# Kernel optimization log

Measured on AMD Instinct MI355X. Metric: run time of the kernel, lower is better.

Reference implementation:

```python
import jax, jax.numpy as jnp
import numpy as np

FEAT_DIM = 2048
HID = 256
N = 1024
NUM_CLASSES = 16
BN_EPS = 1e-5


def _batchnorm(x, gamma, beta):
    # training-mode BatchNorm1d: per-batch mean, biased variance
    m = x.mean(axis=0)
    v = x.var(axis=0)
    return gamma * (x - m) / jnp.sqrt(v + BN_EPS) + beta


def setup_inputs() -> dict:
    key = jax.random.key(0)
    ks = jax.random.split(key, 12)
    s1 = 1.0 / np.sqrt(FEAT_DIM)
    s2 = 1.0 / np.sqrt(HID)
    s3 = 1.0 / np.sqrt(2 * HID)
    return {
        "features": jax.random.normal(ks[0], (N, FEAT_DIM), dtype=jnp.float32),
        "labels": jax.random.randint(ks[1], (N,), 0, NUM_CLASSES, dtype=jnp.int32),
        # semantic disentangler
        "W1": jax.random.normal(ks[2], (FEAT_DIM, HID), dtype=jnp.float32) * s1,
        "b1": jnp.zeros((HID,), jnp.float32),
        "g1": jnp.ones((HID,), jnp.float32),
        "bt1": jnp.zeros((HID,), jnp.float32),
        "W2": jax.random.normal(ks[3], (HID, HID), dtype=jnp.float32) * s2,
        "b2": jnp.zeros((HID,), jnp.float32),
        "g2": jnp.ones((HID,), jnp.float32),
        "bt2": jnp.zeros((HID,), jnp.float32),
        # edge network: Linear(2H -> H), Linear(H -> 1)
        "We1": jax.random.normal(ks[4], (2 * HID, HID), dtype=jnp.float32) * s3,
        "bwe1": jnp.zeros((HID,), jnp.float32),
        "We2": jax.random.normal(ks[5], (HID, 1), dtype=jnp.float32) * s2,
        "bwe2": jnp.zeros((1,), jnp.float32),
    }


def reference(features, labels, W1, b1, g1, bt1, W2, b2, g2, bt2,
              We1, bwe1, We2, bwe2):
    # semantic disentangler: (Linear -> BN -> ReLU) x2
    h = jax.nn.relu(_batchnorm(features @ W1 + b1, g1, bt1))
    di = jax.nn.relu(_batchnorm(h @ W2 + b2, g2, bt2))  # [N, H]

    # EdgeNetwork all-pairs: Linear on concat([f_i, f_j]) splits into two GEMMs
    hi = di @ We1[:HID]   # [N, H] contribution of node i (first half of concat)
    hj = di @ We1[HID:]   # [N, H] contribution of node j (second half)
    pair = jax.nn.relu(hi[:, None, :] + hj[None, :, :] + bwe1)  # [N, N, H]
    logits = pair @ We2[:, 0] + bwe2[0]                          # [N, N]
    same_label = labels[:, None] == labels[None, :]
    off_diag = ~jnp.eye(N, dtype=bool)
    edge_weights = jnp.where(same_label & off_diag,
                             jax.nn.sigmoid(logits), 0.0)        # [N, N]

    # update_node_features: f_i + sum_j w_ij f_j / sum_j w_ij (if wsum > 0)
    weighted_sum = edge_weights @ di                 # [N, H] (w_ii == 0)
    wsum = edge_weights.sum(axis=1, keepdims=True)   # [N, 1]
    denom = jnp.where(wsum > 0, wsum, 1.0)
    updated = di + jnp.where(wsum > 0, weighted_sum / denom, 0.0)
    return updated
```

## Files before the change

### kernel.cpp

```cpp
#include <hip/hip_runtime.h>
#include <math.h>

#define N_PTS 1024
#define HID   256
#define FEAT  2048

typedef short bf16x8 __attribute__((ext_vector_type(8)));
typedef float f32x4  __attribute__((ext_vector_type(4)));

__device__ inline ushort f2bf(float f) {
    union { float f; unsigned u; } v; v.f = f;
    unsigned r = v.u + 0x7fff + ((v.u >> 16) & 1);
    return (ushort)(r >> 16);
}

__global__ __launch_bounds__(256) void prep(
    const float* __restrict__ features, const float* __restrict__ W1,
    const float* __restrict__ W2, const float* __restrict__ We1,
    ushort* __restrict__ Af, ushort* __restrict__ W1T,
    ushort* __restrict__ W2T, ushort* __restrict__ WeT,
    float* __restrict__ stats)
{
    const int tid = threadIdx.x;
    int b = blockIdx.x;
    if (b < 512) {
        if (b == 300)
            ((float4*)stats)[tid] = make_float4(0.f, 0.f, 0.f, 0.f);
        #pragma unroll
        for (int q = 0; q < 2; q++) {
            const size_t g = (size_t)b * 256 + tid + (size_t)q * 131072;
            float4 v0 = ((const float4*)features)[g * 2];
            float4 v1 = ((const float4*)features)[g * 2 + 1];
            bf16x8 o;
            o[0] = (short)f2bf(v0.x); o[1] = (short)f2bf(v0.y);
            o[2] = (short)f2bf(v0.z); o[3] = (short)f2bf(v0.w);
            o[4] = (short)f2bf(v1.x); o[5] = (short)f2bf(v1.y);
            o[6] = (short)f2bf(v1.z); o[7] = (short)f2bf(v1.w);
            ((bf16x8*)Af)[g] = o;
        }
        return;
    }
    __shared__ ushort Ts[64 * 72];
    const float* src; ushort* dst; int K;
    b -= 512;
    if (b < 128)      { src = W1;  dst = W1T; K = 2048; }
    else if (b < 144) { b -= 128; src = W2;  dst = W2T; K = 256; }
    else              { b -= 144; src = We1; dst = WeT; K = 512; }
    const int k0 = (b >> 2) * 64;
    const int n0 = (b & 3) * 64;
    #pragma unroll
    for (int p = 0; p < 4; p++) {
        const int c  = p * 256 + tid;
        const int r  = c >> 4;
        const int cq = c & 15;
        float4 v = *(const float4*)&src[(size_t)(k0 + r) * 256 + n0 + cq * 4];
        Ts[(cq * 4 + 0) * 72 + r] = f2bf(v.x);
        Ts[(cq * 4 + 1) * 72 + r] = f2bf(v.y);
        Ts[(cq * 4 + 2) * 72 + r] = f2bf(v.z);
        Ts[(cq * 4 + 3) * 72 + r] = f2bf(v.w);
    }
    __syncthreads();
    #pragma unroll
    for (int p = 0; p < 2; p++) {
        const int c    = p * 256 + tid;
        const int row  = c >> 3;
        const int col8 = c & 7;
        *(bf16x8*)&dst[(size_t)(n0 + row) * K + k0 + col8 * 8] =
            *(bf16x8*)&Ts[row * 72 + col8 * 8];
    }
}

__global__ __launch_bounds__(256) void gemm1p(
    const ushort* __restrict__ A, const ushort* __restrict__ B,
    float* __restrict__ Cp)
{
    __shared__ ushort As[64 * 72];
    __shared__ ushort Bs[64 * 72];
    const int tid  = threadIdx.x;
    const int lane = tid & 63;
    const int wave = tid >> 6;
    const int wy = wave >> 1, wx = wave & 1;
    const int quad = lane >> 4, l16 = lane & 15;
    const int mBase = blockIdx.y * 64;
    const int nBase = blockIdx.x * 64;
    const int kBeg  = blockIdx.z * 256;
    float* C = Cp + (size_t)blockIdx.z * (N_PTS * HID);

    f32x4 acc[2][2] = {};
    for (int ks = kBeg; ks < kBeg + 256; ks += 64) {
        #pragma unroll
        for (int p = 0; p < 2; p++) {
            const int c    = p * 256 + tid;
            const int row  = c >> 3;
            const int col8 = c & 7;
            *(bf16x8*)&As[row * 72 + col8 * 8] =
                *(const bf16x8*)&A[(size_t)(mBase + row) * FEAT + ks + col8 * 8];
            *(bf16x8*)&Bs[row * 72 + col8 * 8] =
                *(const bf16x8*)&B[(size_t)(nBase + row) * FEAT + ks + col8 * 8];
        }
        __syncthreads();
        #pragma unroll
        for (int kt = 0; kt < 64; kt += 32) {
            bf16x8 af[2], bfr[2];
            #pragma unroll
            for (int mi = 0; mi < 2; mi++)
                af[mi] = *(bf16x8*)&As[(wy * 32 + mi * 16 + l16) * 72 + kt + quad * 8];
            #pragma unroll
            for (int ni = 0; ni < 2; ni++)
                bfr[ni] = *(bf16x8*)&Bs[(wx * 32 + ni * 16 + l16) * 72 + kt + quad * 8];
            #pragma unroll
            for (int mi = 0; mi < 2; mi++)
                #pragma unroll
                for (int ni = 0; ni < 2; ni++)
                    acc[mi][ni] = __builtin_amdgcn_mfma_f32_16x16x32_bf16(
                        af[mi], bfr[ni], acc[mi][ni], 0, 0, 0);
        }
        __syncthreads();
    }
    #pragma unroll
    for (int mi = 0; mi < 2; mi++)
        #pragma unroll
        for (int ni = 0; ni < 2; ni++)
            #pragma unroll
            for (int e = 0; e < 4; e++) {
                const int gm = mBase + wy * 32 + mi * 16 + quad * 4 + e;
                const int gn = nBase + wx * 32 + ni * 16 + l16;
                C[(size_t)gm * HID + gn] = acc[mi][ni][e];
            }
}

__global__ __launch_bounds__(256) void reduce_stats(
    const float* __restrict__ Xp, float* __restrict__ X,
    float* __restrict__ sum, float* __restrict__ sq)
{
    const int c = threadIdx.x;
    const int r0 = blockIdx.x * 4;
    float s = 0.f, q = 0.f;
    for (int r = r0; r < r0 + 4; ++r) {
        float v = 0.f;
        #pragma unroll
        for (int z = 0; z < 8; z++)
            v += Xp[(size_t)z * (N_PTS * HID) + r * HID + c];
        X[r * HID + c] = v;
        s += v;
        q = fmaf(v, v, q);
    }
    unsafeAtomicAdd(&sum[c], s);
    unsafeAtomicAdd(&sq[c], q);
}

__global__ __launch_bounds__(256) void gemm2_fused(
    const float* __restrict__ A , const ushort* __restrict__ B ,
    float* __restrict__ C ,
    const float* __restrict__ sum1, const float* __restrict__ sq1,
    const float* __restrict__ g1, const float* __restrict__ bt1,
    float* __restrict__ sum2, float* __restrict__ sq2)
{
    __shared__ ushort As[64 * 72];
    __shared__ ushort Bs[64 * 72];
    __shared__ float sscale[HID];
    __shared__ float sshift[HID];
    __shared__ float csum[64];
    __shared__ float csq[64];
    const int tid  = threadIdx.x;
    const int lane = tid & 63;
    const int wave = tid >> 6;
    const int wy = wave >> 1, wx = wave & 1;
    const int quad = lane >> 4, l16 = lane & 15;
    const int mBase = blockIdx.y * 64;
    const int nBase = blockIdx.x * 64;

    {
        float m   = sum1[tid] * (1.f / 1024.f);
        float var = fmaf(-m, m, sq1[tid] * (1.f / 1024.f));
        float rstd = rsqrtf(var + 1e-5f);
        float sc = g1[tid] * rstd;
        sscale[tid] = sc;
        sshift[tid] = fmaf(-m, sc, bt1[tid]);
    }
    if (tid < 64) { csum[tid] = 0.f; csq[tid] = 0.f; }
    __syncthreads();

    f32x4 acc[2][2] = {};
    for (int ks = 0; ks < HID; ks += 64) {
        #pragma unroll
        for (int p = 0; p < 4; p++) {
            const int c  = p * 256 + tid;
            const int r  = c >> 4;
            const int cq = c & 15;
            const int k0 = ks + cq * 4;
            float4 av = *(const float4*)&A[(size_t)(mBase + r) * HID + k0];
            float v0 = fmaxf(fmaf(sscale[k0 + 0], av.x, sshift[k0 + 0]), 0.f);
            float v1 = fmaxf(fmaf(sscale[k0 + 1], av.y, sshift[k0 + 1]), 0.f);
            float v2 = fmaxf(fmaf(sscale[k0 + 2], av.z, sshift[k0 + 2]), 0.f);
            float v3 = fmaxf(fmaf(sscale[k0 + 3], av.w, sshift[k0 + 3]), 0.f);
            ushort4 ao;
            ao.x = f2bf(v0); ao.y = f2bf(v1); ao.z = f2bf(v2); ao.w = f2bf(v3);
            *(ushort4*)&As[r * 72 + cq * 4] = ao;
        }
        #pragma unroll
        for (int p = 0; p < 2; p++) {
            const int c    = p * 256 + tid;
            const int row  = c >> 3;
            const int col8 = c & 7;
            *(bf16x8*)&Bs[row * 72 + col8 * 8] =
                *(const bf16x8*)&B[(size_t)(nBase + row) * HID + ks + col8 * 8];
        }
        __syncthreads();
        #pragma unroll
        for (int kt = 0; kt < 64; kt += 32) {
            bf16x8 af[2], bfr[2];
            #pragma unroll
            for (int mi = 0; mi < 2; mi++)
                af[mi] = *(bf16x8*)&As[(wy * 32 + mi * 16 + l16) * 72 + kt + quad * 8];
            #pragma unroll
            for (int ni = 0; ni < 2; ni++)
                bfr[ni] = *(bf16x8*)&Bs[(wx * 32 + ni * 16 + l16) * 72 + kt + quad * 8];
            #pragma unroll
            for (int mi = 0; mi < 2; mi++)
                #pragma unroll
                for (int ni = 0; ni < 2; ni++)
                    acc[mi][ni] = __builtin_amdgcn_mfma_f32_16x16x32_bf16(
                        af[mi], bfr[ni], acc[mi][ni], 0, 0, 0);
        }
        __syncthreads();
    }

    float s[2] = {0.f, 0.f}, q[2] = {0.f, 0.f};
    #pragma unroll
    for (int mi = 0; mi < 2; mi++)
        #pragma unroll
        for (int ni = 0; ni < 2; ni++)
            #pragma unroll
            for (int e = 0; e < 4; e++) {
                const int gm = mBase + wy * 32 + mi * 16 + quad * 4 + e;
                const int gn = nBase + wx * 32 + ni * 16 + l16;
                float v = acc[mi][ni][e];
                C[(size_t)gm * HID + gn] = v;
                s[ni] += v;
                q[ni] = fmaf(v, v, q[ni]);
            }
    #pragma unroll
    for (int ni = 0; ni < 2; ni++) {
        float sv = s[ni], qv = q[ni];
        sv += __shfl_xor(sv, 16, 64); sv += __shfl_xor(sv, 32, 64);
        qv += __shfl_xor(qv, 16, 64); qv += __shfl_xor(qv, 32, 64);
        if (quad == 0) {
            atomicAdd(&csum[wx * 32 + ni * 16 + l16], sv);
            atomicAdd(&csq [wx * 32 + ni * 16 + l16], qv);
        }
    }
    __syncthreads();
    if (tid < 64) {
        unsafeAtomicAdd(&sum2[nBase + tid], csum[tid]);
        unsafeAtomicAdd(&sq2 [nBase + tid], csq[tid]);
    }
}

__global__ __launch_bounds__(256) void gemm_dual_bn(
    const float* __restrict__ A , const ushort* __restrict__ WeT,
    float* __restrict__ C1 , float* __restrict__ C2 ,
    const float* __restrict__ sum2, const float* __restrict__ sq2,
    const float* __restrict__ g2, const float* __restrict__ bt2,
    float* __restrict__ di)
{
    __shared__ ushort As[64 * 72];
    __shared__ ushort Bs[64 * 72];
    __shared__ float sscale[HID];
    __shared__ float sshift[HID];
    const int tid  = threadIdx.x;
    const int lane = tid & 63;
    const int wave = tid >> 6;
    const int wy = wave >> 1, wx = wave & 1;
    const int quad = lane >> 4, l16 = lane & 15;
    const int mBase = blockIdx.y * 64;
    const int nBase = blockIdx.x * 64;
    const int half  = blockIdx.z;
    float* C = half ? C2 : C1;
    const bool writeDi = (blockIdx.x == 0) && (half == 0);

    {
        float m   = sum2[tid] * (1.f / 1024.f);
        float var = fmaf(-m, m, sq2[tid] * (1.f / 1024.f));
        float rstd = rsqrtf(var + 1e-5f);
        float sc = g2[tid] * rstd;
        sscale[tid] = sc;
        sshift[tid] = fmaf(-m, sc, bt2[tid]);
    }
    __syncthreads();

    f32x4 acc[2][2] = {};
    for (int ks = 0; ks < HID; ks += 64) {
        #pragma unroll
        for (int p = 0; p < 4; p++) {
            const int c  = p * 256 + tid;
            const int r  = c >> 4;
            const int cq = c & 15;
            const int k0 = ks + cq * 4;
            float4 av = *(const float4*)&A[(size_t)(mBase + r) * HID + k0];
            float v0 = fmaxf(fmaf(sscale[k0 + 0], av.x, sshift[k0 + 0]), 0.f);
            float v1 = fmaxf(fmaf(sscale[k0 + 1], av.y, sshift[k0 + 1]), 0.f);
            float v2 = fmaxf(fmaf(sscale[k0 + 2], av.z, sshift[k0 + 2]), 0.f);
            float v3 = fmaxf(fmaf(sscale[k0 + 3], av.w, sshift[k0 + 3]), 0.f);
            if (writeDi)
                *(float4*)&di[(size_t)(mBase + r) * HID + k0] =
                    make_float4(v0, v1, v2, v3);
            ushort4 ao;
            ao.x = f2bf(v0); ao.y = f2bf(v1); ao.z = f2bf(v2); ao.w = f2bf(v3);
            *(ushort4*)&As[r * 72 + cq * 4] = ao;
        }
        #pragma unroll
        for (int p = 0; p < 2; p++) {
            const int c    = p * 256 + tid;
            const int row  = c >> 3;
            const int col8 = c & 7;
            *(bf16x8*)&Bs[row * 72 + col8 * 8] =
                *(const bf16x8*)&WeT[(size_t)(nBase + row) * 512 + half * 256 + ks + col8 * 8];
        }
        __syncthreads();
        #pragma unroll
        for (int kt = 0; kt < 64; kt += 32) {
            bf16x8 af[2], bfr[2];
            #pragma unroll
            for (int mi = 0; mi < 2; mi++)
                af[mi] = *(bf16x8*)&As[(wy * 32 + mi * 16 + l16) * 72 + kt + quad * 8];
            #pragma unroll
            for (int ni = 0; ni < 2; ni++)
                bfr[ni] = *(bf16x8*)&Bs[(wx * 32 + ni * 16 + l16) * 72 + kt + quad * 8];
            #pragma unroll
            for (int mi = 0; mi < 2; mi++)
                #pragma unroll
                for (int ni = 0; ni < 2; ni++)
                    acc[mi][ni] = __builtin_amdgcn_mfma_f32_16x16x32_bf16(
                        af[mi], bfr[ni], acc[mi][ni], 0, 0, 0);
        }
        __syncthreads();
    }
    #pragma unroll
    for (int mi = 0; mi < 2; mi++)
        #pragma unroll
        for (int ni = 0; ni < 2; ni++)
            #pragma unroll
            for (int e = 0; e < 4; e++) {
                const int gm = mBase + wy * 32 + mi * 16 + quad * 4 + e;
                const int gn = nBase + wx * 32 + ni * 16 + l16;
                C[(size_t)gm * HID + gn] = acc[mi][ni][e];
            }
}

__global__ __launch_bounds__(256) void pair_update2(
    const float* __restrict__ di, const float* __restrict__ hi,
    const float* __restrict__ hj, const float* __restrict__ bwe1,
    const float* __restrict__ We2, const float* __restrict__ bwe2,
    const int* __restrict__ labels, float* __restrict__ out)
{
    __shared__ int   slab[N_PTS];
    __shared__ int   list[N_PTS];
    __shared__ int   cnt;
    __shared__ float sacc[16][HID];
    __shared__ float swsum[16];
    const int i   = blockIdx.x;
    const int tid = threadIdx.x;
    const int pid = tid >> 4;
    const int l16 = tid & 15;

    if (tid == 0) cnt = 0;
    for (int t = tid; t < N_PTS; t += 256) slab[t] = labels[t];
    __syncthreads();
    const int myLab = slab[i];
    for (int t = tid; t < N_PTS; t += 256)
        if (slab[t] == myLab && t != i) list[atomicAdd(&cnt, 1)] = t;
    __syncthreads();
    const int n = cnt;

    const float4* hip4 = (const float4*)(hi + (size_t)i * HID) + l16 * 4;
    const float4* bw4  = (const float4*)bwe1 + l16 * 4;
    const float4* w24  = (const float4*)We2  + l16 * 4;
    float4 hb[4], w2[4];
    #pragma unroll
    for (int s = 0; s < 4; s++) {
        float4 a = hip4[s], b = bw4[s];
        hb[s] = make_float4(a.x + b.x, a.y + b.y, a.z + b.z, a.w + b.w);
        w2[s] = w24[s];
    }
    const float b2 = bwe2[0];

    float4 acc[4] = {};
    float wloc = 0.f;
    const int rounds = (n + 15) >> 4;
    for (int r = 0; r < rounds; ++r) {
        const int idx = r * 16 + pid;
        const bool valid = idx < n;
        const int jj = valid ? list[idx] : i;
        const float4* hv4 = (const float4*)(hj + (size_t)jj * HID) + l16 * 4;
        float4 hv[4];
        #pragma unroll
        for (int s = 0; s < 4; s++) hv[s] = hv4[s];
        float p = 0.f;
        #pragma unroll
        for (int s = 0; s < 4; s++) {
            p = fmaf(fmaxf(hb[s].x + hv[s].x, 0.f), w2[s].x, p);
            p = fmaf(fmaxf(hb[s].y + hv[s].y, 0.f), w2[s].y, p);
            p = fmaf(fmaxf(hb[s].z + hv[s].z, 0.f), w2[s].z, p);
            p = fmaf(fmaxf(hb[s].w + hv[s].w, 0.f), w2[s].w, p);
        }
        p += __shfl_xor(p, 1, 64);
        p += __shfl_xor(p, 2, 64);
        p += __shfl_xor(p, 4, 64);
        p += __shfl_xor(p, 8, 64);
        const float w = valid ? 1.f / (1.f + expf(-(p + b2))) : 0.f;
        const float4* dv4 = (const float4*)(di + (size_t)jj * HID) + l16 * 4;
        #pragma unroll
        for (int s = 0; s < 4; s++) {
            float4 d = dv4[s];
            acc[s].x = fmaf(w, d.x, acc[s].x);
            acc[s].y = fmaf(w, d.y, acc[s].y);
            acc[s].z = fmaf(w, d.z, acc[s].z);
            acc[s].w = fmaf(w, d.w, acc[s].w);
        }
        if (l16 == 0) wloc += w;
    }
    #pragma unroll
    for (int s = 0; s < 4; s++)
        ((float4*)&sacc[pid][l16 * 16])[s] = acc[s];
    if (l16 == 0) swsum[pid] = wloc;
    __syncthreads();

    float at = 0.f;
    #pragma unroll
    for (int g = 0; g < 16; g++) at += sacc[g][tid];
    float wt = 0.f;
    #pragma unroll
    for (int g = 0; g < 16; g++) wt += swsum[g];
    const float dval = di[(size_t)i * HID + tid];
    out[(size_t)i * HID + tid] = dval + (wt > 0.f ? at / wt : 0.f);
}

extern "C" void kernel_launch(void* const* d_in, const int* in_sizes, int n_in,
                              void* d_out, int out_size, void* d_ws, size_t ws_size,
                              hipStream_t stream)
{
    const float* features = (const float*)d_in[0];
    const int*   labels   = (const int*)d_in[1];
    const float* W1   = (const float*)d_in[2];
    const float* g1   = (const float*)d_in[4];
    const float* bt1  = (const float*)d_in[5];
    const float* W2   = (const float*)d_in[6];
    const float* g2   = (const float*)d_in[8];
    const float* bt2  = (const float*)d_in[9];
    const float* We1  = (const float*)d_in[10];
    const float* bwe1 = (const float*)d_in[11];
    const float* We2  = (const float*)d_in[12];
    const float* bwe2 = (const float*)d_in[13];
    float* out = (float*)d_out;

    float* ws    = (float*)d_ws;
    float* x1    = ws;
    float* hi    = ws + 262144;
    float* hj    = ws + 524288;
    float* stats = ws + 786432;
    float* x2    = ws + 787456;
    float* di    = ws + 1049600;
    float* x1p   = ws + 1311744;
    ushort* Af   = (ushort*)(ws + 3408896);
    ushort* W1T  = Af + 2097152;
    ushort* W2T  = W1T + 524288;
    ushort* WeT  = W2T + 65536;

    dim3 blk(256);
    prep<<<688, blk, 0, stream>>>(features, W1, W2, We1, Af, W1T, W2T, WeT,
                                  stats);
    gemm1p<<<dim3(4, 16, 8), blk, 0, stream>>>(Af, W1T, x1p);
    reduce_stats<<<256, blk, 0, stream>>>(x1p, x1, stats, stats + 256);
    gemm2_fused<<<dim3(4, 16, 1), blk, 0, stream>>>(x1, W2T, x2,
                                                    stats, stats + 256, g1, bt1,
                                                    stats + 512, stats + 768);
    gemm_dual_bn<<<dim3(4, 16, 2), blk, 0, stream>>>(x2, WeT, hi, hj,
                                                     stats + 512, stats + 768,
                                                     g2, bt2, di);
    pair_update2<<<N_PTS, blk, 0, stream>>>(di, hi, hj, bwe1, We2, bwe2,
                                            labels, out);
}
```

Baseline: 138.4 us.

## Fuse all stages into one persistent kernel with software grid barriers

Replaces the six separate kernel launches with a single persistent 512-block kernel. Stages are separated by an atomic-counter grid barrier, and the counter is reset with a memset before each launch. This is meant to remove per-launch overhead and the gaps between dependent kernels. In exchange, several stages now run on only a subset of blocks while the rest sit idle. The barrier also needs every block to be co-resident, and its spin loop has a timeout that could silently break correctness if that does not hold.

```diff
diff --git a/kernel.cpp b/kernel.cpp
--- a/kernel.cpp
+++ b/kernel.cpp
@@ -4,6 +4,7 @@
 #define N_PTS 1024
 #define HID   256
 #define FEAT  2048
+#define GRID  512
 
 typedef short bf16x8 __attribute__((ext_vector_type(8)));
 typedef float f32x4  __attribute__((ext_vector_type(4)));
@@ -14,21 +15,60 @@
     return (ushort)(r >> 16);
 }
 
-__global__ __launch_bounds__(256) void prep(
-    const float* __restrict__ features, const float* __restrict__ W1,
-    const float* __restrict__ W2, const float* __restrict__ We1,
-    ushort* __restrict__ Af, ushort* __restrict__ W1T,
-    ushort* __restrict__ W2T, ushort* __restrict__ WeT,
-    float* __restrict__ stats)
+__device__ __forceinline__ void gridbar(unsigned* cnt, unsigned target) {
+    __syncthreads();
+    if (threadIdx.x == 0) {
+        __threadfence();
+        __hip_atomic_fetch_add(cnt, 1u, __ATOMIC_ACQ_REL,
+                               __HIP_MEMORY_SCOPE_AGENT);
+        unsigned spins = 0;
+        while (__hip_atomic_load(cnt, __ATOMIC_ACQUIRE,
+                                 __HIP_MEMORY_SCOPE_AGENT) < target) {
+            __builtin_amdgcn_s_sleep(2);
+            if (++spins > (1u << 22)) break;
+        }
+        __threadfence();
+    }
+    __syncthreads();
+}
+
+__global__ __launch_bounds__(256, 2) void fused_all(
+    const float* __restrict__ features, const int* __restrict__ labels,
+    const float* __restrict__ W1, const float* __restrict__ g1,
+    const float* __restrict__ bt1, const float* __restrict__ W2,
+    const float* __restrict__ g2, const float* __restrict__ bt2,
+    const float* __restrict__ We1, const float* __restrict__ bwe1,
+    const float* __restrict__ We2, const float* __restrict__ bwe2,
+    float* __restrict__ out, float* __restrict__ ws)
 {
-    const int tid = threadIdx.x;
-    int b = blockIdx.x;
-    if (b < 512) {
-        if (b == 300)
+    __shared__ __align__(16) unsigned char smem[24704];
+
+    float* x1    = ws;
+    float* hi    = ws + 262144;
+    float* hj    = ws + 524288;
+    float* stats = ws + 786432;
+    float* x2    = ws + 787456;
+    float* di    = ws + 1049600;
+    float* x1p   = ws + 1311744;
+    ushort* Af   = (ushort*)(ws + 3408896);
+    ushort* W1T  = Af + 2097152;
+    ushort* W2T  = W1T + 524288;
+    ushort* WeT  = W2T + 65536;
+    unsigned* bar = (unsigned*)(ws + 4817920);
+
+    const int tid  = threadIdx.x;
+    const int bid  = blockIdx.x;
+    const int lane = tid & 63;
+    const int wave = tid >> 6;
+    const int wy = wave >> 1, wx = wave & 1;
+    const int quad = lane >> 4, l16 = lane & 15;
+
+    {
+        if (bid == 300)
             ((float4*)stats)[tid] = make_float4(0.f, 0.f, 0.f, 0.f);
         #pragma unroll
         for (int q = 0; q < 2; q++) {
-            const size_t g = (size_t)b * 256 + tid + (size_t)q * 131072;
+            const size_t g = (size_t)bid * 256 + tid + (size_t)q * 131072;
             float4 v0 = ((const float4*)features)[g * 2];
             float4 v1 = ((const float4*)features)[g * 2 + 1];
             bf16x8 o;
@@ -38,402 +78,369 @@
             o[6] = (short)f2bf(v1.z); o[7] = (short)f2bf(v1.w);
             ((bf16x8*)Af)[g] = o;
         }
-        return;
-    }
-    __shared__ ushort Ts[64 * 72];
-    const float* src; ushort* dst; int K;
-    b -= 512;
-    if (b < 128)      { src = W1;  dst = W1T; K = 2048; }
-    else if (b < 144) { b -= 128; src = W2;  dst = W2T; K = 256; }
-    else              { b -= 144; src = We1; dst = WeT; K = 512; }
-    const int k0 = (b >> 2) * 64;
-    const int n0 = (b & 3) * 64;
-    #pragma unroll
-    for (int p = 0; p < 4; p++) {
-        const int c  = p * 256 + tid;
-        const int r  = c >> 4;
-        const int cq = c & 15;
-        float4 v = *(const float4*)&src[(size_t)(k0 + r) * 256 + n0 + cq * 4];
-        Ts[(cq * 4 + 0) * 72 + r] = f2bf(v.x);
-        Ts[(cq * 4 + 1) * 72 + r] = f2bf(v.y);
-        Ts[(cq * 4 + 2) * 72 + r] = f2bf(v.z);
-        Ts[(cq * 4 + 3) * 72 + r] = f2bf(v.w);
-    }
-    __syncthreads();
-    #pragma unroll
-    for (int p = 0; p < 2; p++) {
-        const int c    = p * 256 + tid;
-        const int row  = c >> 3;
-        const int col8 = c & 7;
-        *(bf16x8*)&dst[(size_t)(n0 + row) * K + k0 + col8 * 8] =
-            *(bf16x8*)&Ts[row * 72 + col8 * 8];
-    }
-}
-
-__global__ __launch_bounds__(256) void gemm1p(
-    const ushort* __restrict__ A, const ushort* __restrict__ B,
-    float* __restrict__ Cp)
-{
-    __shared__ ushort As[64 * 72];
-    __shared__ ushort Bs[64 * 72];
-    const int tid  = threadIdx.x;
-    const int lane = tid & 63;
-    const int wave = tid >> 6;
-    const int wy = wave >> 1, wx = wave & 1;
-    const int quad = lane >> 4, l16 = lane & 15;
-    const int mBase = blockIdx.y * 64;
-    const int nBase = blockIdx.x * 64;
-    const int kBeg  = blockIdx.z * 256;
-    float* C = Cp + (size_t)blockIdx.z * (N_PTS * HID);
-
-    f32x4 acc[2][2] = {};
-    for (int ks = kBeg; ks < kBeg + 256; ks += 64) {
-        #pragma unroll
-        for (int p = 0; p < 2; p++) {
-            const int c    = p * 256 + tid;
-            const int row  = c >> 3;
-            const int col8 = c & 7;
-            *(bf16x8*)&As[row * 72 + col8 * 8] =
-                *(const bf16x8*)&A[(size_t)(mBase + row) * FEAT + ks + col8 * 8];
-            *(bf16x8*)&Bs[row * 72 + col8 * 8] =
-                *(const bf16x8*)&B[(size_t)(nBase + row) * FEAT + ks + col8 * 8];
-        }
+        if (bid < 176) {
+            ushort* Ts = (ushort*)smem;
+            int b = bid; const float* src; ushort* dst; int K;
+            if (b < 128)      { src = W1;  dst = W1T; K = 2048; }
+            else if (b < 144) { b -= 128; src = W2;  dst = W2T; K = 256; }
+            else              { b -= 144; src = We1; dst = WeT; K = 512; }
+            const int k0 = (b >> 2) * 64;
+            const int n0 = (b & 3) * 64;
+            #pragma unroll
+            for (int p = 0; p < 4; p++) {
+                const int c  = p * 256 + tid;
+                const int r  = c >> 4;
+                const int cq = c & 15;
+                float4 v = *(const float4*)&src[(size_t)(k0 + r) * 256 + n0 + cq * 4];
+                Ts[(cq * 4 + 0) * 72 + r] = f2bf(v.x);
+                Ts[(cq * 4 + 1) * 72 + r] = f2bf(v.y);
+                Ts[(cq * 4 + 2) * 72 + r] = f2bf(v.z);
+                Ts[(cq * 4 + 3) * 72 + r] = f2bf(v.w);
+            }
+            __syncthreads();
+            #pragma unroll
+            for (int p = 0; p < 2; p++) {
+                const int c    = p * 256 + tid;
+                const int row  = c >> 3;
+                const int col8 = c & 7;
+                *(bf16x8*)&dst[(size_t)(n0 + row) * K + k0 + col8 * 8] =
+                    *(bf16x8*)&Ts[row * 72 + col8 * 8];
+            }
+        }
+    }
+    gridbar(bar, 1 * GRID);
+
+    {
+        ushort* As = (ushort*)smem;
+        ushort* Bs = (ushort*)(smem + 9216);
+        const int x = bid & 3, y = (bid >> 2) & 15, z = bid >> 6;
+        const int mBase = y * 64, nBase = x * 64, kBeg = z * 256;
+        float* C = x1p + (size_t)z * (N_PTS * HID);
+        f32x4 acc[2][2] = {};
+        for (int ks = kBeg; ks < kBeg + 256; ks += 64) {
+            #pragma unroll
+            for (int p = 0; p < 2; p++) {
+                const int c    = p * 256 + tid;
+                const int row  = c >> 3;
+                const int col8 = c & 7;
+                *(bf16x8*)&As[row * 72 + col8 * 8] =
+                    *(const bf16x8*)&Af[(size_t)(mBase + row) * FEAT + ks + col8 * 8];
+                *(bf16x8*)&Bs[row * 72 + col8 * 8] =
+                    *(const bf16x8*)&W1T[(size_t)(nBase + row) * FEAT + ks + col8 * 8];
+            }
+            __syncthreads();
+            #pragma unroll
+            for (int kt = 0; kt < 64; kt += 32) {
+                bf16x8 af[2], bfr[2];
+                #pragma unroll
+                for (int mi = 0; mi < 2; mi++)
+                    af[mi] = *(bf16x8*)&As[(wy * 32 + mi * 16 + l16) * 72 + kt + quad * 8];
+                #pragma unroll
+                for (int ni = 0; ni < 2; ni++)
+                    bfr[ni] = *(bf16x8*)&Bs[(wx * 32 + ni * 16 + l16) * 72 + kt + quad * 8];
+                #pragma unroll
+                for (int mi = 0; mi < 2; mi++)
+                    #pragma unroll
+                    for (int ni = 0; ni < 2; ni++)
+                        acc[mi][ni] = __builtin_amdgcn_mfma_f32_16x16x32_bf16(
+                            af[mi], bfr[ni], acc[mi][ni], 0, 0, 0);
+            }
+            __syncthreads();
+        }
+        #pragma unroll
+        for (int mi = 0; mi < 2; mi++)
+            #pragma unroll
+            for (int ni = 0; ni < 2; ni++)
+                #pragma unroll
+                for (int e = 0; e < 4; e++) {
+                    const int gm = mBase + wy * 32 + mi * 16 + quad * 4 + e;
+                    const int gn = nBase + wx * 32 + ni * 16 + l16;
+                    C[(size_t)gm * HID + gn] = acc[mi][ni][e];
+                }
+    }
+    gridbar(bar, 2 * GRID);
+
+    if (bid < 256) {
+        const int c = tid;
+        const int r0 = bid * 4;
+        float s = 0.f, q = 0.f;
+        for (int r = r0; r < r0 + 4; ++r) {
+            float v = 0.f;
+            #pragma unroll
+            for (int z = 0; z < 8; z++)
+                v += x1p[(size_t)z * (N_PTS * HID) + r * HID + c];
+            x1[r * HID + c] = v;
+            s += v;
+            q = fmaf(v, v, q);
+        }
+        unsafeAtomicAdd(&stats[c], s);
+        unsafeAtomicAdd(&stats[256 + c], q);
+    }
+    gridbar(bar, 3 * GRID);
+
+    if (bid < 64) {
+        ushort* As = (ushort*)smem;
+        ushort* Bs = (ushort*)(smem + 9216);
+        float* sscale = (float*)(smem + 18432);
+        float* sshift = (float*)(smem + 19456);
+        float* csum   = (float*)(smem + 20480);
+        float* csq    = (float*)(smem + 20736);
+        const int x = bid & 3, y = bid >> 2;
+        const int mBase = y * 64, nBase = x * 64;
+        {
+            float m   = stats[tid] * (1.f / 1024.f);
+            float var = fmaf(-m, m, stats[256 + tid] * (1.f / 1024.f));
+            float rstd = rsqrtf(var + 1e-5f);
+            float sc = g1[tid] * rstd;
+            sscale[tid] = sc;
+            sshift[tid] = fmaf(-m, sc, bt1[tid]);
+        }
+        if (tid < 64) { csum[tid] = 0.f; csq[tid] = 0.f; }
         __syncthreads();
-        #pragma unroll
-        for (int kt = 0; kt < 64; kt += 32) {
-            bf16x8 af[2], bfr[2];
-            #pragma unroll
-            for (int mi = 0; mi < 2; mi++)
-                af[mi] = *(bf16x8*)&As[(wy * 32 + mi * 16 + l16) * 72 + kt + quad * 8];
+
+        f32x4 acc[2][2] = {};
+        for (int ks = 0; ks < HID; ks += 64) {
+            #pragma unroll
+            for (int p = 0; p < 4; p++) {
+                const int c  = p * 256 + tid;
+                const int r  = c >> 4;
+                const int cq = c & 15;
+                const int k0 = ks + cq * 4;
+                float4 av = *(const float4*)&x1[(size_t)(mBase + r) * HID + k0];
+                float v0 = fmaxf(fmaf(sscale[k0 + 0], av.x, sshift[k0 + 0]), 0.f);
+                float v1 = fmaxf(fmaf(sscale[k0 + 1], av.y, sshift[k0 + 1]), 0.f);
+                float v2 = fmaxf(fmaf(sscale[k0 + 2], av.z, sshift[k0 + 2]), 0.f);
+                float v3 = fmaxf(fmaf(sscale[k0 + 3], av.w, sshift[k0 + 3]), 0.f);
+                ushort4 ao;
+                ao.x = f2bf(v0); ao.y = f2bf(v1); ao.z = f2bf(v2); ao.w = f2bf(v3);
+                *(ushort4*)&As[r * 72 + cq * 4] = ao;
+            }
+            #pragma unroll
+            for (int p = 0; p < 2; p++) {
+                const int c    = p * 256 + tid;
+                const int row  = c >> 3;
+                const int col8 = c & 7;
+                *(bf16x8*)&Bs[row * 72 + col8 * 8] =
+                    *(const bf16x8*)&W2T[(size_t)(nBase + row) * HID + ks + col8 * 8];
+            }
+            __syncthreads();
+            #pragma unroll
+            for (int kt = 0; kt < 64; kt += 32) {
+                bf16x8 af[2], bfr[2];
+                #pragma unroll
+                for (int mi = 0; mi < 2; mi++)
+                    af[mi] = *(bf16x8*)&As[(wy * 32 + mi * 16 + l16) * 72 + kt + quad * 8];
+                #pragma unroll
+                for (int ni = 0; ni < 2; ni++)
+                    bfr[ni] = *(bf16x8*)&Bs[(wx * 32 + ni * 16 + l16) * 72 + kt + quad * 8];
+                #pragma unroll
+                for (int mi = 0; mi < 2; mi++)
+                    #pragma unroll
+                    for (int ni = 0; ni < 2; ni++)
+                        acc[mi][ni] = __builtin_amdgcn_mfma_f32_16x16x32_bf16(
+                            af[mi], bfr[ni], acc[mi][ni], 0, 0, 0);
+            }
+            __syncthreads();
+        }
+        float s[2] = {0.f, 0.f}, q[2] = {0.f, 0.f};
+        #pragma unroll
+        for (int mi = 0; mi < 2; mi++)
             #pragma unroll
             for (int ni = 0; ni < 2; ni++)
-                bfr[ni] = *(bf16x8*)&Bs[(wx * 32 + ni * 16 + l16) * 72 + kt + quad * 8];
-            #pragma unroll
-            for (int mi = 0; mi < 2; mi++)
+                #pragma unroll
+                for (int e = 0; e < 4; e++) {
+                    const int gm = mBase + wy * 32 + mi * 16 + quad * 4 + e;
+                    const int gn = nBase + wx * 32 + ni * 16 + l16;
+                    float v = acc[mi][ni][e];
+                    x2[(size_t)gm * HID + gn] = v;
+                    s[ni] += v;
+                    q[ni] = fmaf(v, v, q[ni]);
+                }
+        #pragma unroll
+        for (int ni = 0; ni < 2; ni++) {
+            float sv = s[ni], qv = q[ni];
+            sv += __shfl_xor(sv, 16, 64); sv += __shfl_xor(sv, 32, 64);
+            qv += __shfl_xor(qv, 16, 64); qv += __shfl_xor(qv, 32, 64);
+            if (quad == 0) {
+                atomicAdd(&csum[wx * 32 + ni * 16 + l16], sv);
+                atomicAdd(&csq [wx * 32 + ni * 16 + l16], qv);
+            }
+        }
+        __syncthreads();
+        if (tid < 64) {
+            unsafeAtomicAdd(&stats[512 + nBase + tid], csum[tid]);
+            unsafeAtomicAdd(&stats[768 + nBase + tid], csq[tid]);
+        }
+    }
+    gridbar(bar, 4 * GRID);
+
+    if (bid < 128) {
+        ushort* As = (ushort*)smem;
+        ushort* Bs = (ushort*)(smem + 9216);
+        float* sscale = (float*)(smem + 18432);
+        float* sshift = (float*)(smem + 19456);
+        const int x = bid & 3, y = (bid >> 2) & 15, half = bid >> 6;
+        const int mBase = y * 64, nBase = x * 64;
+        float* C = half ? hj : hi;
+        const bool writeDi = (x == 0) && (half == 0);
+        {
+            float m   = stats[512 + tid] * (1.f / 1024.f);
+            float var = fmaf(-m, m, stats[768 + tid] * (1.f / 1024.f));
+            float rstd = rsqrtf(var + 1e-5f);
+            float sc = g2[tid] * rstd;
+            sscale[tid] = sc;
+            sshift[tid] = fmaf(-m, sc, bt2[tid]);
+        }
+        __syncthreads();
+
+        f32x4 acc[2][2] = {};
+        for (int ks = 0; ks < HID; ks += 64) {
+            #pragma unroll
+            for (int p = 0; p < 4; p++) {
+                const int c  = p * 256 + tid;
+                const int r  = c >> 4;
+                const int cq = c & 15;
+                const int k0 = ks + cq * 4;
+                float4 av = *(const float4*)&x2[(size_t)(mBase + r) * HID + k0];
+                float v0 = fmaxf(fmaf(sscale[k0 + 0], av.x, sshift[k0 + 0]), 0.f);
+                float v1 = fmaxf(fmaf(sscale[k0 + 1], av.y, sshift[k0 + 1]), 0.f);
+                float v2 = fmaxf(fmaf(sscale[k0 + 2], av.z, sshift[k0 + 2]), 0.f);
+                float v3 = fmaxf(fmaf(sscale[k0 + 3], av.w, sshift[k0 + 3]), 0.f);
+                if (writeDi)
+                    *(float4*)&di[(size_t)(mBase + r) * HID + k0] =
+                        make_float4(v0, v1, v2, v3);
+                ushort4 ao;
+                ao.x = f2bf(v0); ao.y = f2bf(v1); ao.z = f2bf(v2); ao.w = f2bf(v3);
+                *(ushort4*)&As[r * 72 + cq * 4] = ao;
+            }
+            #pragma unroll
+            for (int p = 0; p < 2; p++) {
+                const int c    = p * 256 + tid;
+                const int row  = c >> 3;
+                const int col8 = c & 7;
+                *(bf16x8*)&Bs[row * 72 + col8 * 8] =
+                    *(const bf16x8*)&WeT[(size_t)(nBase + row) * 512 + half * 256 + ks + col8 * 8];
+            }
+            __syncthreads();
+            #pragma unroll
+            for (int kt = 0; kt < 64; kt += 32) {
+                bf16x8 af[2], bfr[2];
+                #pragma unroll
+                for (int mi = 0; mi < 2; mi++)
+                    af[mi] = *(bf16x8*)&As[(wy * 32 + mi * 16 + l16) * 72 + kt + quad * 8];
                 #pragma unroll
                 for (int ni = 0; ni < 2; ni++)
-                    acc[mi][ni] = __builtin_amdgcn_mfma_f32_16x16x32_bf16(
-                        af[mi], bfr[ni], acc[mi][ni], 0, 0, 0);
-        }
-        __syncthreads();
-    }
-    #pragma unroll
-    for (int mi = 0; mi < 2; mi++)
-        #pragma unroll
-        for (int ni = 0; ni < 2; ni++)
-            #pragma unroll
-            for (int e = 0; e < 4; e++) {
-                const int gm = mBase + wy * 32 + mi * 16 + quad * 4 + e;
-                const int gn = nBase + wx * 32 + ni * 16 + l16;
-                C[(size_t)gm * HID + gn] = acc[mi][ni][e];
-            }
-}
-
-__global__ __launch_bounds__(256) void reduce_stats(
-    const float* __restrict__ Xp, float* __restrict__ X,
-    float* __restrict__ sum, float* __restrict__ sq)
-{
-    const int c = threadIdx.x;
-    const int r0 = blockIdx.x * 4;
-    float s = 0.f, q = 0.f;
-    for (int r = r0; r < r0 + 4; ++r) {
-        float v = 0.f;
-        #pragma unroll
-        for (int z = 0; z < 8; z++)
-            v += Xp[(size_t)z * (N_PTS * HID) + r * HID + c];
-        X[r * HID + c] = v;
-        s += v;
-        q = fmaf(v, v, q);
-    }
-    unsafeAtomicAdd(&sum[c], s);
-    unsafeAtomicAdd(&sq[c], q);
-}
-
-__global__ __launch_bounds__(256) void gemm2_fused(
-    const float* __restrict__ A , const ushort* __restrict__ B ,
-    float* __restrict__ C ,
-    const float* __restrict__ sum1, const float* __restrict__ sq1,
-    const float* __restrict__ g1, const float* __restrict__ bt1,
-    float* __restrict__ sum2, float* __restrict__ sq2)
-{
-    __shared__ ushort As[64 * 72];
-    __shared__ ushort Bs[64 * 72];
-    __shared__ float sscale[HID];
-    __shared__ float sshift[HID];
-    __shared__ float csum[64];
-    __shared__ float csq[64];
-    const int tid  = threadIdx.x;
-    const int lane = tid & 63;
-    const int wave = tid >> 6;
-    const int wy = wave >> 1, wx = wave & 1;
-    const int quad = lane >> 4, l16 = lane & 15;
-    const int mBase = blockIdx.y * 64;
-    const int nBase = blockIdx.x * 64;
+                    bfr[ni] = *(bf16x8*)&Bs[(wx * 32 + ni * 16 + l16) * 72 + kt + quad * 8];
+                #pragma unroll
+                for (int mi = 0; mi < 2; mi++)
+                    #pragma unroll
+                    for (int ni = 0; ni < 2; ni++)
+                        acc[mi][ni] = __builtin_amdgcn_mfma_f32_16x16x32_bf16(
+                            af[mi], bfr[ni], acc[mi][ni], 0, 0, 0);
+            }
+            __syncthreads();
+        }
+        #pragma unroll
+        for (int mi = 0; mi < 2; mi++)
+            #pragma unroll
+            for (int ni = 0; ni < 2; ni++)
+                #pragma unroll
+                for (int e = 0; e < 4; e++) {
+                    const int gm = mBase + wy * 32 + mi * 16 + quad * 4 + e;
+                    const int gn = nBase + wx * 32 + ni * 16 + l16;
+                    C[(size_t)gm * HID + gn] = acc[mi][ni][e];
+                }
+    }
+    gridbar(bar, 5 * GRID);
 
     {
-        float m   = sum1[tid] * (1.f / 1024.f);
-        float var = fmaf(-m, m, sq1[tid] * (1.f / 1024.f));
-        float rstd = rsqrtf(var + 1e-5f);
-        float sc = g1[tid] * rstd;
-        sscale[tid] = sc;
-        sshift[tid] = fmaf(-m, sc, bt1[tid]);
-    }
-    if (tid < 64) { csum[tid] = 0.f; csq[tid] = 0.f; }
-    __syncthreads();
-
-    f32x4 acc[2][2] = {};
-    for (int ks = 0; ks < HID; ks += 64) {
-        #pragma unroll
-        for (int p = 0; p < 4; p++) {
-            const int c  = p * 256 + tid;
-            const int r  = c >> 4;
-            const int cq = c & 15;
-            const int k0 = ks + cq * 4;
-            float4 av = *(const float4*)&A[(size_t)(mBase + r) * HID + k0];
-            float v0 = fmaxf(fmaf(sscale[k0 + 0], av.x, sshift[k0 + 0]), 0.f);
-            float v1 = fmaxf(fmaf(sscale[k0 + 1], av.y, sshift[k0 + 1]), 0.f);
-            float v2 = fmaxf(fmaf(sscale[k0 + 2], av.z, sshift[k0 + 2]), 0.f);
-            float v3 = fmaxf(fmaf(sscale[k0 + 3], av.w, sshift[k0 + 3]), 0.f);
-            ushort4 ao;
-            ao.x = f2bf(v0); ao.y = f2bf(v1); ao.z = f2bf(v2); ao.w = f2bf(v3);
-            *(ushort4*)&As[r * 72 + cq * 4] = ao;
-        }
-        #pragma unroll
-        for (int p = 0; p < 2; p++) {
-            const int c    = p * 256 + tid;
-            const int row  = c >> 3;
-            const int col8 = c & 7;
-            *(bf16x8*)&Bs[row * 72 + col8 * 8] =
-                *(const bf16x8*)&B[(size_t)(nBase + row) * HID + ks + col8 * 8];
-        }
-        __syncthreads();
-        #pragma unroll
-        for (int kt = 0; kt < 64; kt += 32) {
-            bf16x8 af[2], bfr[2];
-            #pragma unroll
-            for (int mi = 0; mi < 2; mi++)
-                af[mi] = *(bf16x8*)&As[(wy * 32 + mi * 16 + l16) * 72 + kt + quad * 8];
-            #pragma unroll
-            for (int ni = 0; ni < 2; ni++)
-                bfr[ni] = *(bf16x8*)&Bs[(wx * 32 + ni * 16 + l16) * 72 + kt + quad * 8];
-            #pragma unroll
-            for (int mi = 0; mi < 2; mi++)
-                #pragma unroll
-                for (int ni = 0; ni < 2; ni++)
-                    acc[mi][ni] = __builtin_amdgcn_mfma_f32_16x16x32_bf16(
-                        af[mi], bfr[ni], acc[mi][ni], 0, 0, 0);
-        }
-        __syncthreads();
-    }
-
-    float s[2] = {0.f, 0.f}, q[2] = {0.f, 0.f};
-    #pragma unroll
-    for (int mi = 0; mi < 2; mi++)
-        #pragma unroll
-        for (int ni = 0; ni < 2; ni++)
-            #pragma unroll
-            for (int e = 0; e < 4; e++) {
-                const int gm = mBase + wy * 32 + mi * 16 + quad * 4 + e;
-                const int gn = nBase + wx * 32 + ni * 16 + l16;
-                float v = acc[mi][ni][e];
-                C[(size_t)gm * HID + gn] = v;
-                s[ni] += v;
-                q[ni] = fmaf(v, v, q[ni]);
-            }
-    #pragma unroll
-    for (int ni = 0; ni < 2; ni++) {
-        float sv = s[ni], qv = q[ni];
-        sv += __shfl_xor(sv, 16, 64); sv += __shfl_xor(sv, 32, 64);
-        qv += __shfl_xor(qv, 16, 64); qv += __shfl_xor(qv, 32, 64);
-        if (quad == 0) {
-            atomicAdd(&csum[wx * 32 + ni * 16 + l16], sv);
-            atomicAdd(&csq [wx * 32 + ni * 16 + l16], qv);
-        }
-    }
-    __syncthreads();
-    if (tid < 64) {
-        unsafeAtomicAdd(&sum2[nBase + tid], csum[tid]);
-        unsafeAtomicAdd(&sq2 [nBase + tid], csq[tid]);
-    }
-}
-
-__global__ __launch_bounds__(256) void gemm_dual_bn(
-    const float* __restrict__ A , const ushort* __restrict__ WeT,
-    float* __restrict__ C1 , float* __restrict__ C2 ,
-    const float* __restrict__ sum2, const float* __restrict__ sq2,
-    const float* __restrict__ g2, const float* __restrict__ bt2,
-    float* __restrict__ di)
-{
-    __shared__ ushort As[64 * 72];
-    __shared__ ushort Bs[64 * 72];
-    __shared__ float sscale[HID];
-    __shared__ float sshift[HID];
-    const int tid  = threadIdx.x;
-    const int lane = tid & 63;
-    const int wave = tid >> 6;
-    const int wy = wave >> 1, wx = wave & 1;
-    const int quad = lane >> 4, l16 = lane & 15;
-    const int mBase = blockIdx.y * 64;
-    const int nBase = blockIdx.x * 64;
-    const int half  = blockIdx.z;
-    float* C = half ? C2 : C1;
-    const bool writeDi = (blockIdx.x == 0) && (half == 0);
-
-    {
-        float m   = sum2[tid] * (1.f / 1024.f);
-        float var = fmaf(-m, m, sq2[tid] * (1.f / 1024.f));
-        float rstd = rsqrtf(var + 1e-5f);
-        float sc = g2[tid] * rstd;
-        sscale[tid] = sc;
-        sshift[tid] = fmaf(-m, sc, bt2[tid]);
-    }
-    __syncthreads();
-
-    f32x4 acc[2][2] = {};
-    for (int ks = 0; ks < HID; ks += 64) {
-        #pragma unroll
-        for (int p = 0; p < 4; p++) {
-            const int c  = p * 256 + tid;
-            const int r  = c >> 4;
-            const int cq = c & 15;
-            const int k0 = ks + cq * 4;
-            float4 av = *(const float4*)&A[(size_t)(mBase + r) * HID + k0];
-            float v0 = fmaxf(fmaf(sscale[k0 + 0], av.x, sshift[k0 + 0]), 0.f);
-            float v1 = fmaxf(fmaf(sscale[k0 + 1], av.y, sshift[k0 + 1]), 0.f);
-            float v2 = fmaxf(fmaf(sscale[k0 + 2], av.z, sshift[k0 + 2]), 0.f);
-            float v3 = fmaxf(fmaf(sscale[k0 + 3], av.w, sshift[k0 + 3]), 0.f);
-            if (writeDi)
-                *(float4*)&di[(size_t)(mBase + r) * HID + k0] =
-                    make_float4(v0, v1, v2, v3);
-            ushort4 ao;
-            ao.x = f2bf(v0); ao.y = f2bf(v1); ao.z = f2bf(v2); ao.w = f2bf(v3);
-            *(ushort4*)&As[r * 72 + cq * 4] = ao;
-        }
-        #pragma unroll
-        for (int p = 0; p < 2; p++) {
-            const int c    = p * 256 + tid;
-            const int row  = c >> 3;
-            const int col8 = c & 7;
-            *(bf16x8*)&Bs[row * 72 + col8 * 8] =
-                *(const bf16x8*)&WeT[(size_t)(nBase + row) * 512 + half * 256 + ks + col8 * 8];
-        }
-        __syncthreads();
-        #pragma unroll
-        for (int kt = 0; kt < 64; kt += 32) {
-            bf16x8 af[2], bfr[2];
-            #pragma unroll
-            for (int mi = 0; mi < 2; mi++)
-                af[mi] = *(bf16x8*)&As[(wy * 32 + mi * 16 + l16) * 72 + kt + quad * 8];
-            #pragma unroll
-            for (int ni = 0; ni < 2; ni++)
-                bfr[ni] = *(bf16x8*)&Bs[(wx * 32 + ni * 16 + l16) * 72 + kt + quad * 8];
-            #pragma unroll
-            for (int mi = 0; mi < 2; mi++)
-                #pragma unroll
-                for (int ni = 0; ni < 2; ni++)
-                    acc[mi][ni] = __builtin_amdgcn_mfma_f32_16x16x32_bf16(
-                        af[mi], bfr[ni], acc[mi][ni], 0, 0, 0);
-        }
-        __syncthreads();
-    }
-    #pragma unroll
-    for (int mi = 0; mi < 2; mi++)
-        #pragma unroll
-        for (int ni = 0; ni < 2; ni++)
-            #pragma unroll
-            for (int e = 0; e < 4; e++) {
-                const int gm = mBase + wy * 32 + mi * 16 + quad * 4 + e;
-                const int gn = nBase + wx * 32 + ni * 16 + l16;
-                C[(size_t)gm * HID + gn] = acc[mi][ni][e];
-            }
-}
-
-__global__ __launch_bounds__(256) void pair_update2(
-    const float* __restrict__ di, const float* __restrict__ hi,
-    const float* __restrict__ hj, const float* __restrict__ bwe1,
-    const float* __restrict__ We2, const float* __restrict__ bwe2,
-    const int* __restrict__ labels, float* __restrict__ out)
-{
-    __shared__ int   slab[N_PTS];
-    __shared__ int   list[N_PTS];
-    __shared__ int   cnt;
-    __shared__ float sacc[16][HID];
-    __shared__ float swsum[16];
-    const int i   = blockIdx.x;
-    const int tid = threadIdx.x;
-    const int pid = tid >> 4;
-    const int l16 = tid & 15;
-
-    if (tid == 0) cnt = 0;
-    for (int t = tid; t < N_PTS; t += 256) slab[t] = labels[t];
-    __syncthreads();
-    const int myLab = slab[i];
-    for (int t = tid; t < N_PTS; t += 256)
-        if (slab[t] == myLab && t != i) list[atomicAdd(&cnt, 1)] = t;
-    __syncthreads();
-    const int n = cnt;
-
-    const float4* hip4 = (const float4*)(hi + (size_t)i * HID) + l16 * 4;
-    const float4* bw4  = (const float4*)bwe1 + l16 * 4;
-    const float4* w24  = (const float4*)We2  + l16 * 4;
-    float4 hb[4], w2[4];
-    #pragma unroll
-    for (int s = 0; s < 4; s++) {
-        float4 a = hip4[s], b = bw4[s];
-        hb[s] = make_float4(a.x + b.x, a.y + b.y, a.z + b.z, a.w + b.w);
-        w2[s] = w24[s];
-    }
-    const float b2 = bwe2[0];
-
-    float4 acc[4] = {};
-    float wloc = 0.f;
-    const int rounds = (n + 15) >> 4;
-    for (int r = 0; r < rounds; ++r) {
-        const int idx = r * 16 + pid;
-        const bool valid = idx < n;
-        const int jj = valid ? list[idx] : i;
-        const float4* hv4 = (const float4*)(hj + (size_t)jj * HID) + l16 * 4;
-        float4 hv[4];
-        #pragma unroll
-        for (int s = 0; s < 4; s++) hv[s] = hv4[s];
-        float p = 0.f;
-        #pragma unroll
-        for (int s = 0; s < 4; s++) {
-            p = fmaf(fmaxf(hb[s].x + hv[s].x, 0.f), w2[s].x, p);
-            p = fmaf(fmaxf(hb[s].y + hv[s].y, 0.f), w2[s].y, p);
-            p = fmaf(fmaxf(hb[s].z + hv[s].z, 0.f), w2[s].z, p);
-            p = fmaf(fmaxf(hb[s].w + hv[s].w, 0.f), w2[s].w, p);
-        }
-        p += __shfl_xor(p, 1, 64);
-        p += __shfl_xor(p, 2, 64);
-        p += __shfl_xor(p, 4, 64);
-        p += __shfl_xor(p, 8, 64);
-        const float w = valid ? 1.f / (1.f + expf(-(p + b2))) : 0.f;
-        const float4* dv4 = (const float4*)(di + (size_t)jj * HID) + l16 * 4;
-        #pragma unroll
-        for (int s = 0; s < 4; s++) {
-            float4 d = dv4[s];
-            acc[s].x = fmaf(w, d.x, acc[s].x);
-            acc[s].y = fmaf(w, d.y, acc[s].y);
-            acc[s].z = fmaf(w, d.z, acc[s].z);
-            acc[s].w = fmaf(w, d.w, acc[s].w);
-        }
-        if (l16 == 0) wloc += w;
-    }
-    #pragma unroll
-    for (int s = 0; s < 4; s++)
-        ((float4*)&sacc[pid][l16 * 16])[s] = acc[s];
-    if (l16 == 0) swsum[pid] = wloc;
-    __syncthreads();
-
-    float at = 0.f;
-    #pragma unroll
-    for (int g = 0; g < 16; g++) at += sacc[g][tid];
-    float wt = 0.f;
-    #pragma unroll
-    for (int g = 0; g < 16; g++) wt += swsum[g];
-    const float dval = di[(size_t)i * HID + tid];
-    out[(size_t)i * HID + tid] = dval + (wt > 0.f ? at / wt : 0.f);
+        int*   slab  = (int*)smem;
+        int*   list  = (int*)(smem + 4096);
+        float (*sacc)[HID] = (float(*)[HID])(smem + 8192);
+        float* swsum = (float*)(smem + 24576);
+        int*   cnt   = (int*)(smem + 24640);
+        const int pid = tid >> 4;
+        const int lq  = tid & 15;
+
+        for (int t = tid; t < N_PTS; t += 256) slab[t] = labels[t];
+
+        const float4* bw4 = (const float4*)bwe1 + lq * 4;
+        const float4* w24 = (const float4*)We2  + lq * 4;
+        float4 bwv[4], w2v[4];
+        #pragma unroll
+        for (int s = 0; s < 4; s++) { bwv[s] = bw4[s]; w2v[s] = w24[s]; }
+        const float b2 = bwe2[0];
+
+        for (int i = bid; i < N_PTS; i += GRID) {
+            if (tid == 0) *cnt = 0;
+            __syncthreads();
+            const int myLab = slab[i];
+            for (int t = tid; t < N_PTS; t += 256)
+                if (slab[t] == myLab && t != i) list[atomicAdd(cnt, 1)] = t;
+            __syncthreads();
+            const int n = *cnt;
+
+            const float4* hip4 = (const float4*)(hi + (size_t)i * HID) + lq * 4;
+            float4 hb[4];
+            #pragma unroll
+            for (int s = 0; s < 4; s++) {
+                float4 a = hip4[s];
+                hb[s] = make_float4(a.x + bwv[s].x, a.y + bwv[s].y,
+                                    a.z + bwv[s].z, a.w + bwv[s].w);
+            }
+
+            float4 acc4[4] = {};
+            float wloc = 0.f;
+            const int rounds = (n + 15) >> 4;
+            for (int r = 0; r < rounds; ++r) {
+                const int idx = r * 16 + pid;
+                const bool valid = idx < n;
+                const int jj = valid ? list[idx] : i;
+                const float4* hv4 = (const float4*)(hj + (size_t)jj * HID) + lq * 4;
+                float4 hv[4];
+                #pragma unroll
+                for (int s = 0; s < 4; s++) hv[s] = hv4[s];
+                float p = 0.f;
+                #pragma unroll
+                for (int s = 0; s < 4; s++) {
+                    p = fmaf(fmaxf(hb[s].x + hv[s].x, 0.f), w2v[s].x, p);
+                    p = fmaf(fmaxf(hb[s].y + hv[s].y, 0.f), w2v[s].y, p);
+                    p = fmaf(fmaxf(hb[s].z + hv[s].z, 0.f), w2v[s].z, p);
+                    p = fmaf(fmaxf(hb[s].w + hv[s].w, 0.f), w2v[s].w, p);
+                }
+                p += __shfl_xor(p, 1, 64);
+                p += __shfl_xor(p, 2, 64);
+                p += __shfl_xor(p, 4, 64);
+                p += __shfl_xor(p, 8, 64);
+                const float w = valid ? 1.f / (1.f + expf(-(p + b2))) : 0.f;
+                const float4* dv4 = (const float4*)(di + (size_t)jj * HID) + lq * 4;
+                #pragma unroll
+                for (int s = 0; s < 4; s++) {
+                    float4 d = dv4[s];
+                    acc4[s].x = fmaf(w, d.x, acc4[s].x);
+                    acc4[s].y = fmaf(w, d.y, acc4[s].y);
+                    acc4[s].z = fmaf(w, d.z, acc4[s].z);
+                    acc4[s].w = fmaf(w, d.w, acc4[s].w);
+                }
+                if (lq == 0) wloc += w;
+            }
+            #pragma unroll
+            for (int s = 0; s < 4; s++)
+                ((float4*)&sacc[pid][lq * 16])[s] = acc4[s];
+            if (lq == 0) swsum[pid] = wloc;
+            __syncthreads();
+
+            float at = 0.f;
+            #pragma unroll
+            for (int g = 0; g < 16; g++) at += sacc[g][tid];
+            float wt = 0.f;
+            #pragma unroll
+            for (int g = 0; g < 16; g++) wt += swsum[g];
+            const float dval = di[(size_t)i * HID + tid];
+            out[(size_t)i * HID + tid] = dval + (wt > 0.f ? at / wt : 0.f);
+            __syncthreads();
+        }
+    }
 }
 
 extern "C" void kernel_launch(void* const* d_in, const int* in_sizes, int n_in,
@@ -453,31 +460,11 @@
     const float* We2  = (const float*)d_in[12];
     const float* bwe2 = (const float*)d_in[13];
     float* out = (float*)d_out;
-
-    float* ws    = (float*)d_ws;
-    float* x1    = ws;
-    float* hi    = ws + 262144;
-    float* hj    = ws + 524288;
-    float* stats = ws + 786432;
-    float* x2    = ws + 787456;
-    float* di    = ws + 1049600;
-    float* x1p   = ws + 1311744;
-    ushort* Af   = (ushort*)(ws + 3408896);
-    ushort* W1T  = Af + 2097152;
-    ushort* W2T  = W1T + 524288;
-    ushort* WeT  = W2T + 65536;
-
-    dim3 blk(256);
-    prep<<<688, blk, 0, stream>>>(features, W1, W2, We1, Af, W1T, W2T, WeT,
-                                  stats);
-    gemm1p<<<dim3(4, 16, 8), blk, 0, stream>>>(Af, W1T, x1p);
-    reduce_stats<<<256, blk, 0, stream>>>(x1p, x1, stats, stats + 256);
-    gemm2_fused<<<dim3(4, 16, 1), blk, 0, stream>>>(x1, W2T, x2,
-                                                    stats, stats + 256, g1, bt1,
-                                                    stats + 512, stats + 768);
-    gemm_dual_bn<<<dim3(4, 16, 2), blk, 0, stream>>>(x2, WeT, hi, hj,
-                                                     stats + 512, stats + 768,
-                                                     g2, bt2, di);
-    pair_update2<<<N_PTS, blk, 0, stream>>>(di, hi, hj, bwe1, We2, bwe2,
-                                            labels, out);
+    float* ws  = (float*)d_ws;
+
+    hipMemsetAsync((char*)d_ws + (size_t)4817920 * 4, 0, 64, stream);
+
+    fused_all<<<dim3(GRID), dim3(256), 0, stream>>>(
+        features, labels, W1, g1, bt1, W2, g2, bt2,
+        We1, bwe1, We2, bwe2, out, ws);
 }
```

Measured after the change: 464.2 us. 235% more time.
